# Optimization experiments

Measured on AMD Instinct MI355X. Metric: run time of the kernel, lower is better.

The kernel has to match this reference:

```python
import jax, jax.numpy as jnp
import numpy as np

B, T, N, FIN, FOUT, EDIM = 2, 32, 64, 64, 64, 16
EPS = 1e-5

def _xavier(key, fan_in, fan_out):
    limit = np.sqrt(6.0 / (fan_in + fan_out))
    return jax.random.uniform(key, (fan_in, fan_out), minval=-limit, maxval=limit, dtype=jnp.float32)

def setup_inputs() -> dict:
    key = jax.random.key(0)
    ks = jax.random.split(key, 8)
    x = jax.random.normal(ks[0], (B, T, N, FIN), dtype=jnp.float32)
    adj = jax.random.uniform(ks[1], (B, N, N), dtype=jnp.float32)
    # edge_net: Linear(1->EDIM), GELU, Linear(EDIM->FIN*FOUT); stored as (in,out)
    ew1 = _xavier(ks[2], 1, EDIM)
    eb1 = jnp.zeros((EDIM,), jnp.float32)
    ew2 = _xavier(ks[3], EDIM, FIN * FOUT)
    eb2 = jnp.zeros((FIN * FOUT,), jnp.float32)
    # node_lin: Linear(FIN->FOUT)
    nw = _xavier(ks[4], FIN, FOUT)
    nb = jnp.zeros((FOUT,), jnp.float32)
    # GraphNorm params (pre_norm -> num_features = FIN)
    gw = jnp.ones((FIN,), jnp.float32)
    gb = jnp.zeros((FIN,), jnp.float32)
    gms = jnp.ones((1,), jnp.float32)
    return {"x": x, "adj": adj, "ew1": ew1, "eb1": eb1, "ew2": ew2, "eb2": eb2,
            "nw": nw, "nb": nb, "gw": gw, "gb": gb, "gms": gms}

def reference(x, adj, ew1, eb1, ew2, eb2, nw, nb, gw, gb, gms):
    # GraphNorm over node axis (dim=-2), pre-norm
    mean = jnp.mean(x, axis=-2, keepdims=True)
    var = jnp.var(x, axis=-2, keepdims=True)  # unbiased=False
    xn = (x - mean * gms) / jnp.sqrt(var + EPS)
    xn = xn * gw + gb  # (B,T,N,FIN)
    # edge-conditioned weights: scalar adj -> (B,N,N,FIN,FOUT)
    ef = adj[..., None]  # (B,N,N,1)
    h = jax.nn.gelu(ef @ ew1 + eb1, approximate=False)  # (B,N,N,EDIM)
    edge_w = (h @ ew2 + eb2).reshape(adj.shape[0], N, N, FIN, FOUT)
    # agg[b,t,i,o] = sum_j sum_f xn[b,t,j,f] * edge_w[b,i,j,f,o]
    agg = jnp.einsum('btjf,bijfo->btio', xn, edge_w)
    y = xn @ nw + nb + agg
    y = jax.nn.gelu(y, approximate=False)  # torch nn.GELU default = exact erf
    return y
```

## Files before the change

kernel.cpp:

```cpp
#include <hip/hip_runtime.h>


#define LSTR 72
#define XSTR 68

typedef unsigned short u16;
typedef _Float16 f16;
typedef _Float16 f16x8 __attribute__((ext_vector_type(8)));
typedef _Float16 f16x4 __attribute__((ext_vector_type(4)));
typedef float f32x4 __attribute__((ext_vector_type(4)));

__device__ __forceinline__ float bf2f(u16 u) {
    union { unsigned int i; float f; } c; c.i = ((unsigned int)u) << 16; return c.f;
}
__device__ __forceinline__ u16 f2bf(float f) {
    union { float f; unsigned int i; } c; c.f = f;
    unsigned int r = c.i + 0x7FFFu + ((c.i >> 16) & 1u);
    return (u16)(r >> 16);
}
__device__ __forceinline__ float gelu_exact(float v) {
    return 0.5f * v * (1.0f + erff(v * 0.70710678118654752440f));
}
__device__ __forceinline__ float loadf(const void* p, int i, bool bf) {
    return bf ? bf2f(((const u16*)p)[i]) : ((const float*)p)[i];
}
__device__ __forceinline__ int detect_bf16(const void* xp) {
    const u16* u = (const u16*)xp;
    int sane = 0;
    for (int k = 0; k < 64; ++k) {
        int e = (u[k * 2] >> 7) & 0xFF;
        sane += (e >= 100 && e <= 150);
    }
    return sane >= 40;
}

__global__ __launch_bounds__(256) void precomp(
    const void* __restrict__ adj, const void* __restrict__ ew1, const void* __restrict__ eb1,
    const void* __restrict__ ew2, const void* __restrict__ nw, const void* __restrict__ x,
    f16* __restrict__ H, f16* __restrict__ W2t, f16* __restrict__ NWt)
{
    __shared__ int s_bf;
    if (threadIdx.x == 0) s_bf = detect_bf16(x);
    __syncthreads();
    const bool bf = (s_bf != 0);

    int idx = blockIdx.x * 256 + threadIdx.x;
    if (idx < 131072) {
        int b = idx >> 16, rem = idx & 65535, e = rem >> 12, ij = rem & 4095;
        float a = loadf(adj, (b << 12) + ij, bf);
        float v = a * loadf(ew1, e, bf) + loadf(eb1, e, bf);
        H[idx] = (f16)gelu_exact(v);
    } else if (idx < 196608) {
        int k = idx - 131072, e = k >> 12, of = k & 4095, o = of >> 6, f = of & 63;
        W2t[k] = (f16)loadf(ew2, (e << 12) + (f << 6) + o, bf);
    } else if (idx < 200704) {
        int k = idx - 196608, o = k >> 6, f = k & 63;
        NWt[k] = (f16)loadf(nw, (f << 6) + o, bf);
    }
}

__global__ __launch_bounds__(256) void fused_main(
    const void* __restrict__ x, const void* __restrict__ eb2, const void* __restrict__ nb,
    const void* __restrict__ gw, const void* __restrict__ gb, const void* __restrict__ gms,
    const f16* __restrict__ H, const f16* __restrict__ W2t, const f16* __restrict__ NWt,
    void* __restrict__ out)
{
    __shared__ float xraw[64 * XSTR];
    __shared__ f16 xn_lds[64 * LSTR];
    __shared__ f16 w2t_lds[64 * LSTR];
    __shared__ f16 h_lds[64 * LSTR];
    __shared__ f16 zt_lds[64 * LSTR];
    __shared__ float red1[256];
    __shared__ float red2[256];
    __shared__ float af[64], cf[64], Sv[64], t2o[64];
    __shared__ int s_bf;

    const int tid  = threadIdx.x;
    const int bt   = blockIdx.x;
    const int b    = bt >> 5;
    const int lane = tid & 63;
    const int wave = tid >> 6;
    const int ln   = lane & 15;
    const int q    = lane >> 4;
    const int row  = tid >> 2;
    const int colb = (tid & 3) << 4;

    if (tid == 0) s_bf = detect_bf16(x);
    __syncthreads();
    const bool bf = (s_bf != 0);

    {
        int base = (bt << 12) + (row << 6) + colb;
        if (bf) {
            const uint4* src = (const uint4*)((const u16*)x + base);
            uint4 v0 = src[0], v1 = src[1];
            const u16* p0 = (const u16*)&v0;
            const u16* p1 = (const u16*)&v1;
            #pragma unroll
            for (int k = 0; k < 8; ++k) {
                xraw[row * XSTR + colb + k]     = bf2f(p0[k]);
                xraw[row * XSTR + colb + 8 + k] = bf2f(p1[k]);
            }
        } else {
            const float4* src = (const float4*)((const float*)x + base);
            #pragma unroll
            for (int k = 0; k < 4; ++k) {
                float4 v = src[k];
                xraw[row * XSTR + colb + 4 * k]     = v.x;
                xraw[row * XSTR + colb + 4 * k + 1] = v.y;
                xraw[row * XSTR + colb + 4 * k + 2] = v.z;
                xraw[row * XSTR + colb + 4 * k + 3] = v.w;
            }
        }
    }
    __syncthreads();
    {
        int f = tid & 63, part = tid >> 6;
        float s1 = 0.f, s2 = 0.f;
        #pragma unroll
        for (int r = 0; r < 16; ++r) {
            float v = xraw[(part * 16 + r) * XSTR + f];
            s1 += v; s2 += v * v;
        }
        red1[part * 64 + f] = s1; red2[part * 64 + f] = s2;
    }
    __syncthreads();
    if (tid < 64) {
        float s1 = red1[tid] + red1[64 + tid] + red1[128 + tid] + red1[192 + tid];
        float s2 = red2[tid] + red2[64 + tid] + red2[128 + tid] + red2[192 + tid];
        float mean = s1 * 0.015625f;
        float var  = s2 * 0.015625f - mean * mean;
        float inv  = rsqrtf(var + 1e-5f);
        float gwf = loadf(gw, tid, bf), gbf = loadf(gb, tid, bf), g = loadf(gms, 0, bf);
        float a = inv * gwf;
        af[tid] = a;
        cf[tid] = gbf - mean * g * a;
        Sv[tid] = 64.f * (mean * (1.f - g) * a + gbf);
    }
    __syncthreads();
    {
        #pragma unroll
        for (int k = 0; k < 16; ++k) {
            int col = colb + k;
            xn_lds[row * LSTR + col] = (f16)(xraw[row * XSTR + col] * af[col] + cf[col]);
        }
    }
    {
        int o = tid & 63, part = tid >> 6;
        float s = 0.f;
        #pragma unroll
        for (int r = 0; r < 16; ++r) {
            int f = part * 16 + r;
            s += Sv[f] * loadf(eb2, (f << 6) + o, bf);
        }
        red1[part * 64 + o] = s;
    }
    __syncthreads();
    if (tid < 64)
        t2o[tid] = red1[tid] + red1[64 + tid] + red1[128 + tid] + red1[192 + tid]
                 + loadf(nb, tid, bf);

    f32x4 acc[4];
    #pragma unroll
    for (int i2 = 0; i2 < 4; ++i2) acc[i2] = (f32x4){0.f, 0.f, 0.f, 0.f};

    for (int e = 0; e < 16; ++e) {
        __syncthreads();
        {
            const uint4* s1 = (const uint4*)(W2t + (e << 12) + (row << 6) + colb);
            const uint4* s2 = (const uint4*)(H + ((b * 16 + e) << 12) + (row << 6) + colb);
            uint4 a0 = s1[0], a1 = s1[1], b0 = s2[0], b1 = s2[1];
            *(uint4*)&w2t_lds[row * LSTR + colb]     = a0;
            *(uint4*)&w2t_lds[row * LSTR + colb + 8] = a1;
            *(uint4*)&h_lds[row * LSTR + colb]       = b0;
            *(uint4*)&h_lds[row * LSTR + colb + 8]   = b1;
        }
        __syncthreads();
        #pragma unroll
        for (int tn = 0; tn < 4; ++tn) {
            f32x4 z = {0.f, 0.f, 0.f, 0.f};
            #pragma unroll
            for (int kc = 0; kc < 2; ++kc) {
                f16x8 a  = *(const f16x8*)&xn_lds[(wave * 16 + ln) * LSTR + kc * 32 + q * 8];
                f16x8 bb = *(const f16x8*)&w2t_lds[(tn * 16 + ln) * LSTR + kc * 32 + q * 8];
                z = __builtin_amdgcn_mfma_f32_16x16x32_f16(a, bb, z, 0, 0, 0);
            }
            f16x4 p;
            #pragma unroll
            for (int r = 0; r < 4; ++r) p[r] = (f16)z[r];
            *(f16x4*)&zt_lds[(tn * 16 + ln) * LSTR + wave * 16 + q * 4] = p;
        }
        __syncthreads();
        #pragma unroll
        for (int tn = 0; tn < 4; ++tn) {
            #pragma unroll
            for (int kc = 0; kc < 2; ++kc) {
                f16x8 a  = *(const f16x8*)&h_lds[(wave * 16 + ln) * LSTR + kc * 32 + q * 8];
                f16x8 bb = *(const f16x8*)&zt_lds[(tn * 16 + ln) * LSTR + kc * 32 + q * 8];
                acc[tn] = __builtin_amdgcn_mfma_f32_16x16x32_f16(a, bb, acc[tn], 0, 0, 0);
            }
        }
    }
    __syncthreads();
    {
        const uint4* s1 = (const uint4*)(NWt + (row << 6) + colb);
        uint4 a0 = s1[0], a1 = s1[1];
        *(uint4*)&w2t_lds[row * LSTR + colb]     = a0;
        *(uint4*)&w2t_lds[row * LSTR + colb + 8] = a1;
    }
    __syncthreads();
    #pragma unroll
    for (int tn = 0; tn < 4; ++tn) {
        #pragma unroll
        for (int kc = 0; kc < 2; ++kc) {
            f16x8 a  = *(const f16x8*)&xn_lds[(wave * 16 + ln) * LSTR + kc * 32 + q * 8];
            f16x8 bb = *(const f16x8*)&w2t_lds[(tn * 16 + ln) * LSTR + kc * 32 + q * 8];
            acc[tn] = __builtin_amdgcn_mfma_f32_16x16x32_f16(a, bb, acc[tn], 0, 0, 0);
        }
    }
    {
        if (bf) {
            u16* ob = (u16*)out + (bt << 12);
            #pragma unroll
            for (int tn = 0; tn < 4; ++tn) {
                int o = tn * 16 + ln;
                float add = t2o[o];
                #pragma unroll
                for (int r = 0; r < 4; ++r) {
                    int i = wave * 16 + q * 4 + r;
                    ob[(i << 6) + o] = f2bf(gelu_exact(acc[tn][r] + add));
                }
            }
        } else {
            float* ob = (float*)out + (bt << 12);
            #pragma unroll
            for (int tn = 0; tn < 4; ++tn) {
                int o = tn * 16 + ln;
                float add = t2o[o];
                #pragma unroll
                for (int r = 0; r < 4; ++r) {
                    int i = wave * 16 + q * 4 + r;
                    ob[(i << 6) + o] = gelu_exact(acc[tn][r] + add);
                }
            }
        }
    }
}

extern "C" void kernel_launch(void* const* d_in, const int* in_sizes, int n_in,
                              void* d_out, int out_size, void* d_ws, size_t ws_size,
                              hipStream_t stream) {
    const void* x   = d_in[0];
    const void* adj = d_in[1];
    const void* ew1 = d_in[2];
    const void* eb1 = d_in[3];
    const void* ew2 = d_in[4];
    const void* eb2 = d_in[5];
    const void* nw  = d_in[6];
    const void* nb  = d_in[7];
    const void* gw  = d_in[8];
    const void* gb  = d_in[9];
    const void* gms = d_in[10];

    f16* H   = (f16*)d_ws;
    f16* W2t = H + 131072;
    f16* NWt = W2t + 65536;

    precomp<<<784, 256, 0, stream>>>(adj, ew1, eb1, ew2, nw, x, H, W2t, NWt);
    fused_main<<<64, 256, 0, stream>>>(x, eb2, nb, gw, gb, gms, H, W2t, NWt, d_out);
}
```

Baseline: 96.89 us.

## Split output columns across two blocks and batch edge dims with direct global operands

The main kernel now runs 128 blocks, each handling half of the output features for one (b,t). MFMA operands for W2t, H and NWt are read straight from global memory into registers instead of being staged through LDS. Four edge dimensions are processed per synchronisation round, and two accumulator sets split the K dimension. This is meant to raise GPU occupancy on the large-CU device and cut barriers per edge dimension. In exchange, each block redundantly recomputes the GraphNorm prologue and reads operands uncoalesced from global memory.

New measurement: 95.33 us. Within noise of the previous version (-1.6%).

```diff
diff --git a/kernel.cpp b/kernel.cpp
--- a/kernel.cpp
+++ b/kernel.cpp
@@ -3,6 +3,7 @@
 
 #define LSTR 72
 #define XSTR 68
+#define CE 4
 
 typedef unsigned short u16;
 typedef _Float16 f16;
@@ -67,16 +68,16 @@
 {
     __shared__ float xraw[64 * XSTR];
     __shared__ f16 xn_lds[64 * LSTR];
-    __shared__ f16 w2t_lds[64 * LSTR];
-    __shared__ f16 h_lds[64 * LSTR];
-    __shared__ f16 zt_lds[64 * LSTR];
+    __shared__ f16 zt_lds[CE * 32 * LSTR];
     __shared__ float red1[256];
     __shared__ float red2[256];
     __shared__ float af[64], cf[64], Sv[64], t2o[64];
     __shared__ int s_bf;
 
     const int tid  = threadIdx.x;
-    const int bt   = blockIdx.x;
+    const int blk  = blockIdx.x;
+    const int bt   = blk >> 1;
+    const int half = blk & 1;
     const int b    = bt >> 5;
     const int lane = tid & 63;
     const int wave = tid >> 6;
@@ -159,88 +160,85 @@
     if (tid < 64)
         t2o[tid] = red1[tid] + red1[64 + tid] + red1[128 + tid] + red1[192 + tid]
                  + loadf(nb, tid, bf);
-
-    f32x4 acc[4];
+    __syncthreads();
+
+    f16x8 xa0 = *(const f16x8*)&xn_lds[(wave * 16 + ln) * LSTR + q * 8];
+    f16x8 xa1 = *(const f16x8*)&xn_lds[(wave * 16 + ln) * LSTR + 32 + q * 8];
+
+    f32x4 accA[2], accB[2];
     #pragma unroll
-    for (int i2 = 0; i2 < 4; ++i2) acc[i2] = (f32x4){0.f, 0.f, 0.f, 0.f};
-
-    for (int e = 0; e < 16; ++e) {
+    for (int i2 = 0; i2 < 2; ++i2) {
+        accA[i2] = (f32x4){0.f, 0.f, 0.f, 0.f};
+        accB[i2] = (f32x4){0.f, 0.f, 0.f, 0.f};
+    }
+
+    for (int ec = 0; ec < 16 / CE; ++ec) {
         __syncthreads();
-        {
-            const uint4* s1 = (const uint4*)(W2t + (e << 12) + (row << 6) + colb);
-            const uint4* s2 = (const uint4*)(H + ((b * 16 + e) << 12) + (row << 6) + colb);
-            uint4 a0 = s1[0], a1 = s1[1], b0 = s2[0], b1 = s2[1];
-            *(uint4*)&w2t_lds[row * LSTR + colb]     = a0;
-            *(uint4*)&w2t_lds[row * LSTR + colb + 8] = a1;
-            *(uint4*)&h_lds[row * LSTR + colb]       = b0;
-            *(uint4*)&h_lds[row * LSTR + colb + 8]   = b1;
+        #pragma unroll
+        for (int el = 0; el < CE; ++el) {
+            int e = ec * CE + el;
+            const f16* w2b = W2t + (((e << 6) + (half << 5)) << 6);
+            #pragma unroll
+            for (int tn = 0; tn < 2; ++tn) {
+                const f16* wrow = w2b + ((tn * 16 + ln) << 6);
+                f16x8 b0 = *(const f16x8*)(wrow + q * 8);
+                f16x8 b1 = *(const f16x8*)(wrow + 32 + q * 8);
+                f32x4 z = {0.f, 0.f, 0.f, 0.f};
+                z = __builtin_amdgcn_mfma_f32_16x16x32_f16(xa0, b0, z, 0, 0, 0);
+                z = __builtin_amdgcn_mfma_f32_16x16x32_f16(xa1, b1, z, 0, 0, 0);
+                f16x4 p;
+                #pragma unroll
+                for (int r = 0; r < 4; ++r) p[r] = (f16)z[r];
+                *(f16x4*)&zt_lds[(el * 32 + tn * 16 + ln) * LSTR + wave * 16 + q * 4] = p;
+            }
         }
         __syncthreads();
         #pragma unroll
-        for (int tn = 0; tn < 4; ++tn) {
-            f32x4 z = {0.f, 0.f, 0.f, 0.f};
-            #pragma unroll
-            for (int kc = 0; kc < 2; ++kc) {
-                f16x8 a  = *(const f16x8*)&xn_lds[(wave * 16 + ln) * LSTR + kc * 32 + q * 8];
-                f16x8 bb = *(const f16x8*)&w2t_lds[(tn * 16 + ln) * LSTR + kc * 32 + q * 8];
-                z = __builtin_amdgcn_mfma_f32_16x16x32_f16(a, bb, z, 0, 0, 0);
-            }
-            f16x4 p;
-            #pragma unroll
-            for (int r = 0; r < 4; ++r) p[r] = (f16)z[r];
-            *(f16x4*)&zt_lds[(tn * 16 + ln) * LSTR + wave * 16 + q * 4] = p;
-        }
-        __syncthreads();
-        #pragma unroll
-        for (int tn = 0; tn < 4; ++tn) {
-            #pragma unroll
-            for (int kc = 0; kc < 2; ++kc) {
-                f16x8 a  = *(const f16x8*)&h_lds[(wave * 16 + ln) * LSTR + kc * 32 + q * 8];
-                f16x8 bb = *(const f16x8*)&zt_lds[(tn * 16 + ln) * LSTR + kc * 32 + q * 8];
-                acc[tn] = __builtin_amdgcn_mfma_f32_16x16x32_f16(a, bb, acc[tn], 0, 0, 0);
-            }
-        }
-    }
-    __syncthreads();
-    {
-        const uint4* s1 = (const uint4*)(NWt + (row << 6) + colb);
-        uint4 a0 = s1[0], a1 = s1[1];
-        *(uint4*)&w2t_lds[row * LSTR + colb]     = a0;
-        *(uint4*)&w2t_lds[row * LSTR + colb + 8] = a1;
-    }
-    __syncthreads();
+        for (int el = 0; el < CE; ++el) {
+            int e = ec * CE + el;
+            const f16* hrow = H + (((b * 16 + e) << 12)) + ((wave * 16 + ln) << 6);
+            f16x8 ha0 = *(const f16x8*)(hrow + q * 8);
+            f16x8 ha1 = *(const f16x8*)(hrow + 32 + q * 8);
+            #pragma unroll
+            for (int tn = 0; tn < 2; ++tn) {
+                f16x8 zb0 = *(const f16x8*)&zt_lds[(el * 32 + tn * 16 + ln) * LSTR + q * 8];
+                f16x8 zb1 = *(const f16x8*)&zt_lds[(el * 32 + tn * 16 + ln) * LSTR + 32 + q * 8];
+                accA[tn] = __builtin_amdgcn_mfma_f32_16x16x32_f16(ha0, zb0, accA[tn], 0, 0, 0);
+                accB[tn] = __builtin_amdgcn_mfma_f32_16x16x32_f16(ha1, zb1, accB[tn], 0, 0, 0);
+            }
+        }
+    }
     #pragma unroll
-    for (int tn = 0; tn < 4; ++tn) {
-        #pragma unroll
-        for (int kc = 0; kc < 2; ++kc) {
-            f16x8 a  = *(const f16x8*)&xn_lds[(wave * 16 + ln) * LSTR + kc * 32 + q * 8];
-            f16x8 bb = *(const f16x8*)&w2t_lds[(tn * 16 + ln) * LSTR + kc * 32 + q * 8];
-            acc[tn] = __builtin_amdgcn_mfma_f32_16x16x32_f16(a, bb, acc[tn], 0, 0, 0);
-        }
+    for (int tn = 0; tn < 2; ++tn) {
+        const f16* nrow = NWt + (((half * 32 + tn * 16 + ln)) << 6);
+        f16x8 b0 = *(const f16x8*)(nrow + q * 8);
+        f16x8 b1 = *(const f16x8*)(nrow + 32 + q * 8);
+        accA[tn] = __builtin_amdgcn_mfma_f32_16x16x32_f16(xa0, b0, accA[tn], 0, 0, 0);
+        accB[tn] = __builtin_amdgcn_mfma_f32_16x16x32_f16(xa1, b1, accB[tn], 0, 0, 0);
     }
     {
         if (bf) {
             u16* ob = (u16*)out + (bt << 12);
             #pragma unroll
-            for (int tn = 0; tn < 4; ++tn) {
-                int o = tn * 16 + ln;
+            for (int tn = 0; tn < 2; ++tn) {
+                int o = half * 32 + tn * 16 + ln;
                 float add = t2o[o];
                 #pragma unroll
                 for (int r = 0; r < 4; ++r) {
                     int i = wave * 16 + q * 4 + r;
-                    ob[(i << 6) + o] = f2bf(gelu_exact(acc[tn][r] + add));
+                    ob[(i << 6) + o] = f2bf(gelu_exact(accA[tn][r] + accB[tn][r] + add));
                 }
             }
         } else {
             float* ob = (float*)out + (bt << 12);
             #pragma unroll
-            for (int tn = 0; tn < 4; ++tn) {
-                int o = tn * 16 + ln;
+            for (int tn = 0; tn < 2; ++tn) {
+                int o = half * 32 + tn * 16 + ln;
                 float add = t2o[o];
                 #pragma unroll
                 for (int r = 0; r < 4; ++r) {
                     int i = wave * 16 + q * 4 + r;
-                    ob[(i << 6) + o] = gelu_exact(acc[tn][r] + add);
+                    ob[(i << 6) + o] = gelu_exact(accA[tn][r] + accB[tn][r] + add);
                 }
             }
         }
@@ -267,5 +265,5 @@
     f16* NWt = W2t + 65536;
 
     precomp<<<784, 256, 0, stream>>>(adj, ew1, eb1, ew2, nw, x, H, W2t, NWt);
-    fused_main<<<64, 256, 0, stream>>>(x, eb2, nb, gw, gb, gms, H, W2t, NWt, d_out);
-}
+    fused_main<<<128, 256, 0, stream>>>(x, eb2, nb, gw, gb, gms, H, W2t, NWt, d_out);
+}
```
